# Optimization experiments

Hardware: AMD Instinct MI355X
Metric: run time of the kernel (lower is better)

Reference implementation:

```python
import jax, jax.numpy as jnp
import numpy as np

N, E, IN, H, D = 50000, 800000, 128, 2, 64  # heads=2, head_dim=64, hidden*2 = 128


def setup_inputs() -> dict:
    key = jax.random.key(0)
    ks = jax.random.split(key, 8)
    s = 1.0 / np.sqrt(IN)
    return {
        "x": jax.random.normal(ks[0], (N, IN), dtype=jnp.float32),
        "edge_index": jax.random.randint(ks[1], (2, E), 0, N, dtype=jnp.int64),
        "Wq": jax.random.normal(ks[2], (IN, H * D), dtype=jnp.float32) * s,
        "bq": jnp.zeros((H * D,), jnp.float32),
        "Wk": jax.random.normal(ks[3], (IN, H * D), dtype=jnp.float32) * s,
        "bk": jnp.zeros((H * D,), jnp.float32),
        "Wv": jax.random.normal(ks[4], (IN, H * D), dtype=jnp.float32) * s,
        "bv": jnp.zeros((H * D,), jnp.float32),
        "Wskip": jax.random.normal(ks[5], (IN, H * D), dtype=jnp.float32) * s,
        "bskip": jnp.zeros((H * D,), jnp.float32),
        "Wdec": jax.random.normal(ks[6], (H * D, IN), dtype=jnp.float32) * (1.0 / np.sqrt(H * D)),
        "bdec": jnp.zeros((IN,), jnp.float32),
    }


def reference(x, edge_index, Wq, bq, Wk, bk, Wv, bv, Wskip, bskip, Wdec, bdec):
    n = x.shape[0]
    src, dst = edge_index[0], edge_index[1]  # message flows src -> dst (PyG convention)
    q = (x @ Wq + bq).reshape(n, H, D)
    k = (x @ Wk + bk).reshape(n, H, D)
    v = (x @ Wv + bv).reshape(n, H, D)
    # per-edge multi-head scores [E, H]
    score = jnp.einsum('ehd,ehd->eh', q[dst], k[src]) / jnp.sqrt(jnp.asarray(D, x.dtype))
    # segment softmax over in-edges of each destination node
    m = jax.ops.segment_max(score, dst, num_segments=n)
    m = jnp.where(jnp.isfinite(m), m, jnp.zeros_like(m))  # nodes with no in-edges
    e = jnp.exp(score - m[dst])
    denom = jax.ops.segment_sum(e, dst, num_segments=n) + 1e-16
    alpha = e / denom[dst]                      # [E, H]
    msg = v[src] * alpha[..., None]             # [E, H, D]
    agg = jax.ops.segment_sum(msg, dst, num_segments=n)  # [N, H, D]
    z = agg.reshape(n, H * D) + (x @ Wskip + bskip)       # concat heads + root skip
    x_hat = z @ Wdec + bdec
    return (x_hat, z)
```

## Files before the change

### kernel.cpp

```cpp
#include <hip/hip_runtime.h>
#include <hip/hip_bf16.h>
#include <math.h>

typedef unsigned short u16;
typedef unsigned char u8;
typedef unsigned int u32;
typedef __attribute__((ext_vector_type(8))) short bf16x8;
typedef __attribute__((ext_vector_type(4))) float f32x4;

__device__ __forceinline__ float b2f(u16 u) {
  union { unsigned int i; float f; } x; x.i = ((unsigned int)u) << 16; return x.f;
}
__device__ __forceinline__ u16 f2b(float f) {
  union { float f; unsigned int i; } x; x.f = f;
  unsigned int r = x.i + 0x7FFFu + ((x.i >> 16) & 1u);
  return (u16)(r >> 16);
}
__device__ __forceinline__ float4 cvt4(ushort4 u) {
  return make_float4(b2f(u.x), b2f(u.y), b2f(u.z), b2f(u.w));
}
__device__ __forceinline__ float4 i8x4_to_f4(u32 w) {
  return make_float4((float)((int)(w << 24) >> 24), (float)((int)(w << 16) >> 24),
                     (float)((int)(w << 8) >> 24), (float)((int)w >> 24));
}

#if __has_builtin(__builtin_amdgcn_sdot4)
__device__ __forceinline__ int dot4i8(u32 a, u32 b) {
  return __builtin_amdgcn_sdot4((int)a, (int)b, 0, false);
}
#else
__device__ __forceinline__ int dot4i8(u32 a, u32 b) {
  int s = ((int)(a << 24) >> 24) * ((int)(b << 24) >> 24);
  s += ((int)(a << 16) >> 24) * ((int)(b << 16) >> 24);
  s += ((int)(a << 8) >> 24) * ((int)(b << 8) >> 24);
  s += ((int)a >> 24) * ((int)b >> 24);
  return s;
}
#endif

__device__ __forceinline__ bool ei_is_i64(const int* __restrict__ ei) {
  return (ei[1] | ei[3] | ei[5] | ei[7] | ei[9] | ei[11] | ei[13] | ei[15]) == 0;
}

__global__ __launch_bounds__(256) void wprep_kernel(
    const float* __restrict__ Wq, const float* __restrict__ Wk,
    const float* __restrict__ Wv, const float* __restrict__ Wsk,
    const float* __restrict__ Wd,
    const float* __restrict__ bq, const float* __restrict__ bk,
    const float* __restrict__ bv, const float* __restrict__ bsk,
    const float* __restrict__ bd,
    short* __restrict__ Wt, float* __restrict__ bias,
    int* __restrict__ cnt, int n) {
  int g = blockIdx.x * 256 + threadIdx.x;
  if (g < 5 * 16384) {
    int mat = g >> 14, rem = g & 16383;
    int nn = rem >> 7, kk = rem & 127;
    const float* W = (mat == 0) ? Wq : (mat == 1) ? Wk : (mat == 2) ? Wv
                     : (mat == 3) ? Wsk : Wd;
    float scl = (mat == 0) ? 0.125f : 1.f;
    Wt[g] = (short)f2b(W[kk * 128 + nn] * scl);
  }
  if (g < 5 * 128) {
    int mat = g >> 7, nn = g & 127;
    const float* B = (mat == 0) ? bq : (mat == 1) ? bk : (mat == 2) ? bv
                     : (mat == 3) ? bsk : bd;
    bias[g] = B[nn] * ((mat == 0) ? 0.125f : 1.f);
  }
  if (g < n) cnt[g] = 0;
}

__global__ __launch_bounds__(256) void count_kernel(const int* __restrict__ ei,
                                                    int* __restrict__ cnt,
                                                    u8* __restrict__ rank, int E) {
  int e = blockIdx.x * 256 + threadIdx.x;
  bool f = ei_is_i64(ei);
  if (e < E) {
    int idx = f ? (e << 1) : e;
    int dbase = f ? (E << 1) : E;
    int d = ei[dbase + idx];
    rank[e] = (u8)atomicAdd(&cnt[d], 1);
  }
}

__global__ __launch_bounds__(1024) void scanA_kernel(const int* __restrict__ cnt,
                                                     int* __restrict__ offs,
                                                     int* __restrict__ parts, int n) {
  __shared__ int wsum[16];
  int i = blockIdx.x * 1024 + threadIdx.x;
  int lane = threadIdx.x & 63, wid = threadIdx.x >> 6;
  int v = (i < n) ? cnt[i] : 0;
  int s = v;
#pragma unroll
  for (int off = 1; off < 64; off <<= 1) {
    int t = __shfl_up(s, off, 64);
    if (lane >= off) s += t;
  }
  if (lane == 63) wsum[wid] = s;
  __syncthreads();
  if (threadIdx.x == 0) {
    int acc = 0;
#pragma unroll
    for (int w = 0; w < 16; ++w) { int t = wsum[w]; wsum[w] = acc; acc += t; }
    parts[blockIdx.x] = acc;
  }
  __syncthreads();
  if (i < n) offs[i] = wsum[wid] + (s - v);
}

__global__ __launch_bounds__(1024) void scanC_kernel(int* __restrict__ offs,
                                                     const int* __restrict__ parts,
                                                     int n, int nb) {
  __shared__ int sh[2];
  if (threadIdx.x < 64) {
    int lane = threadIdx.x;
    int v = (lane < nb) ? parts[lane] : 0;
    int s = v;
#pragma unroll
    for (int off = 1; off < 64; off <<= 1) {
      int t = __shfl_up(s, off, 64);
      if (lane >= off) s += t;
    }
    int base = __shfl(s - v, blockIdx.x, 64);
    int tot  = __shfl(s, nb - 1, 64);
    if (lane == 0) { sh[0] = base; sh[1] = tot; }
  }
  __syncthreads();
  int i = blockIdx.x * 1024 + threadIdx.x;
  if (i < n) offs[i] += sh[0];
  if (i == 0) offs[n] = sh[1];
}

__global__ __launch_bounds__(256) void scatter_kernel(const int* __restrict__ ei,
                                                      const int* __restrict__ offs,
                                                      const u8* __restrict__ rank,
                                                      int* __restrict__ csr, int E) {
  int e = blockIdx.x * 256 + threadIdx.x;
  bool f = ei_is_i64(ei);
  if (e < E) {
    int idx = f ? (e << 1) : e;
    int dbase = f ? (E << 1) : E;
    int s = ei[idx];
    int d = ei[dbase + idx];
    int pos = offs[d] + (int)rank[e];
    __builtin_nontemporal_store(s, &csr[pos]);
  }
}

__global__ __launch_bounds__(256) void proj_kernel(const float* __restrict__ x,
    const short* __restrict__ Wt, const float* __restrict__ bias,
    u32* __restrict__ q8, float* __restrict__ qscb,
    u32* __restrict__ kvq, float* __restrict__ scb,
    u16* __restrict__ skipb, int n) {
  __shared__ short xt[32 * 128];
  int m0 = blockIdx.x * 32;
  int tid = threadIdx.x;
#pragma unroll
  for (int p = 0; p < 2; ++p) {
    int cid = tid + p * 256;
    int row = cid >> 4, c = cid & 15;
    int grow = m0 + row;
    bf16x8 val;
    if (grow < n) {
      const float* sp = x + (size_t)grow * 128 + c * 8;
      float4 f0 = *(const float4*)sp;
      float4 f1 = *(const float4*)(sp + 4);
      val[0] = (short)f2b(f0.x); val[1] = (short)f2b(f0.y);
      val[2] = (short)f2b(f0.z); val[3] = (short)f2b(f0.w);
      val[4] = (short)f2b(f1.x); val[5] = (short)f2b(f1.y);
      val[6] = (short)f2b(f1.z); val[7] = (short)f2b(f1.w);
    } else {
#pragma unroll
      for (int j = 0; j < 8; ++j) val[j] = 0;
    }
    *(bf16x8*)&xt[row * 128 + ((c ^ (row & 15)) << 3)] = val;
  }
  __syncthreads();

  int wid = tid >> 6, l = tid & 63;
  int lm = l & 15, lk = l >> 4;
  const short* W = Wt + (size_t)wid * 16384;
  f32x4 acc[2][8];
#pragma unroll
  for (int mt = 0; mt < 2; ++mt)
#pragma unroll
    for (int nt = 0; nt < 8; ++nt) acc[mt][nt] = (f32x4){0.f, 0.f, 0.f, 0.f};

#pragma unroll
  for (int s = 0; s < 4; ++s) {
    bf16x8 bfrag[2];
#pragma unroll
    for (int mt = 0; mt < 2; ++mt) {
      int ml = mt * 16 + lm;
      int c = s * 4 + lk;
      bfrag[mt] = *(const bf16x8*)&xt[ml * 128 + ((c ^ (ml & 15)) << 3)];
    }
#pragma unroll
    for (int nt = 0; nt < 8; ++nt) {
      bf16x8 afrag = *(const bf16x8*)(W + (size_t)(nt * 16 + lm) * 128 + s * 32 + lk * 8);
      acc[0][nt] = __builtin_amdgcn_mfma_f32_16x16x32_bf16(afrag, bfrag[0], acc[0][nt], 0, 0, 0);
      acc[1][nt] = __builtin_amdgcn_mfma_f32_16x16x32_bf16(afrag, bfrag[1], acc[1][nt], 0, 0, 0);
    }
  }

  const float* bs = bias + wid * 128;
  if (wid < 3) {
#pragma unroll
    for (int mt = 0; mt < 2; ++mt) {
      int m = m0 + mt * 16 + lm;
#pragma unroll
      for (int nt = 0; nt < 8; ++nt) {
        float4 b4 = *(const float4*)(bs + nt * 16 + lk * 4);
        acc[mt][nt][0] += b4.x; acc[mt][nt][1] += b4.y;
        acc[mt][nt][2] += b4.z; acc[mt][nt][3] += b4.w;
      }
#pragma unroll
      for (int h = 0; h < 2; ++h) {
        float am = 0.f;
#pragma unroll
        for (int nt4 = 0; nt4 < 4; ++nt4) {
          int nt = h * 4 + nt4;
#pragma unroll
          for (int j = 0; j < 4; ++j) am = fmaxf(am, fabsf(acc[mt][nt][j]));
        }
        am = fmaxf(am, __shfl_xor(am, 16));
        am = fmaxf(am, __shfl_xor(am, 32));
        float inv = (am > 0.f) ? 127.f / am : 0.f;
        if (m < n) {
#pragma unroll
          for (int nt4 = 0; nt4 < 4; ++nt4) {
            int nt = h * 4 + nt4;
            u32 pk = 0;
#pragma unroll
            for (int j = 0; j < 4; ++j) {
              float qv = fminf(fmaxf(rintf(acc[mt][nt][j] * inv), -127.f), 127.f);
              pk |= ((u32)((int)qv & 0xff)) << (8 * j);
            }
            int slot = nt4 * 4 + lk;
            if (wid == 0) q8[(size_t)m * 32 + h * 16 + slot] = pk;
            else kvq[(size_t)m * 64 + h * 32 + slot * 2 + (wid - 1)] = pk;
          }
          if (lk == 0) {
            float sc = am * (1.f / 127.f);
            if (wid == 0) qscb[(size_t)m * 2 + h] = sc;
            else scb[(size_t)m * 4 + h * 2 + (wid - 1)] = sc;
          }
        }
      }
    }
  } else {
#pragma unroll
    for (int mt = 0; mt < 2; ++mt) {
      int m = m0 + mt * 16 + lm;
      if (m >= n) continue;
#pragma unroll
      for (int nt = 0; nt < 8; ++nt) {
        int n4 = nt * 16 + lk * 4;
        float4 b4 = *(const float4*)(bs + n4);
        f32x4 a = acc[mt][nt];
        ushort4 o;
        o.x = f2b(a[0] + b4.x); o.y = f2b(a[1] + b4.y);
        o.z = f2b(a[2] + b4.z); o.w = f2b(a[3] + b4.w);
        *(ushort4*)(skipb + (size_t)m * 128 + n4) = o;
      }
    }
  }
}

__global__ __launch_bounds__(256) void dec_kernel(const float* __restrict__ zin,
    const short* __restrict__ Wt, const float* __restrict__ bias,
    float* __restrict__ out, int n) {
  __shared__ short zt[128 * 128];
  int m0 = blockIdx.x * 128;
  int tid = threadIdx.x;
#pragma unroll
  for (int p = 0; p < 8; ++p) {
    int cid = tid + p * 256;
    int row = cid >> 4, c = cid & 15;
    int grow = m0 + row;
    bf16x8 val;
    if (grow < n) {
      const float* sp = zin + (size_t)grow * 128 + c * 8;
      float4 f0 = *(const float4*)sp;
      float4 f1 = *(const float4*)(sp + 4);
      val[0] = (short)f2b(f0.x); val[1] = (short)f2b(f0.y);
      val[2] = (short)f2b(f0.z); val[3] = (short)f2b(f0.w);
      val[4] = (short)f2b(f1.x); val[5] = (short)f2b(f1.y);
      val[6] = (short)f2b(f1.z); val[7] = (short)f2b(f1.w);
    } else {
#pragma unroll
      for (int j = 0; j < 8; ++j) val[j] = 0;
    }
    *(bf16x8*)&zt[row * 128 + ((c ^ (row & 15)) << 3)] = val;
  }
  __syncthreads();

  int wid = tid >> 6, l = tid & 63;
  int lm = l & 15, lk = l >> 4;
  int mbase = wid * 32;
  f32x4 acc[2][8];
#pragma unroll
  for (int mt = 0; mt < 2; ++mt)
#pragma unroll
    for (int nt = 0; nt < 8; ++nt) acc[mt][nt] = (f32x4){0.f, 0.f, 0.f, 0.f};

#pragma unroll
  for (int s = 0; s < 4; ++s) {
    bf16x8 bfrag[2];
#pragma unroll
    for (int mt = 0; mt < 2; ++mt) {
      int ml = mbase + mt * 16 + lm;
      int c = s * 4 + lk;
      bfrag[mt] = *(const bf16x8*)&zt[ml * 128 + ((c ^ (ml & 15)) << 3)];
    }
#pragma unroll
    for (int nt = 0; nt < 8; ++nt) {
      bf16x8 afrag = *(const bf16x8*)(Wt + (size_t)(nt * 16 + lm) * 128 + s * 32 + lk * 8);
      acc[0][nt] = __builtin_amdgcn_mfma_f32_16x16x32_bf16(afrag, bfrag[0], acc[0][nt], 0, 0, 0);
      acc[1][nt] = __builtin_amdgcn_mfma_f32_16x16x32_bf16(afrag, bfrag[1], acc[1][nt], 0, 0, 0);
    }
  }

#pragma unroll
  for (int mt = 0; mt < 2; ++mt) {
    int m = m0 + mbase + mt * 16 + lm;
    if (m >= n) continue;
#pragma unroll
    for (int nt = 0; nt < 8; ++nt) {
      int n4 = nt * 16 + lk * 4;
      float4 b4 = *(const float4*)(bias + n4);
      f32x4 a = acc[mt][nt];
      *(float4*)(out + (size_t)m * 128 + n4) =
          make_float4(a[0] + b4.x, a[1] + b4.y, a[2] + b4.z, a[3] + b4.w);
    }
  }
}

#define EDGE_BODY(J, SACC, AACC)                                             \
  {                                                                          \
    int pi = dot4i8(qw, x##J.x);                                             \
    pi += __shfl_xor(pi, 1, 16);                                             \
    pi += __shfl_xor(pi, 2, 16);                                             \
    pi += __shfl_xor(pi, 4, 16);                                             \
    pi += __shfl_xor(pi, 8, 16);                                             \
    float w = __expf((float)pi * (qs * c##J.x));                             \
    float4 vv = i8x4_to_f4(x##J.y);                                          \
    float wv = w * c##J.y;                                                   \
    SACC += w;                                                               \
    AACC.x += wv * vv.x; AACC.y += wv * vv.y;                                \
    AACC.z += wv * vv.z; AACC.w += wv * vv.w;                                \
  }

__global__ __launch_bounds__(256) void attn_kernel(const u32* __restrict__ q8,
                                                   const float* __restrict__ qscb,
                                                   const u32* __restrict__ kvq,
                                                   const float* __restrict__ scb,
                                                   const u16* __restrict__ skipb,
                                                   const int* __restrict__ offs,
                                                   const int* __restrict__ csr,
                                                   float* __restrict__ z, int nn) {
  int dst = blockIdx.x * 8 + (threadIdx.x >> 5);
  int lane32 = threadIdx.x & 31;
  int h = lane32 >> 4, l16 = lane32 & 15;
  if (dst >= nn) return;
  u32 qw = q8[(size_t)dst * 32 + h * 16 + l16];
  float qs = qscb[(size_t)dst * 2 + h];
  int i0 = offs[dst], i1 = offs[dst + 1];
  int kvbase = h * 32 + l16 * 2;
  int scbase = h * 2;

  float s0 = 0.f, s1 = 0.f, s2 = 0.f, s3 = 0.f;
  float4 A0 = {0, 0, 0, 0}, A1 = {0, 0, 0, 0}, A2 = {0, 0, 0, 0}, A3 = {0, 0, 0, 0};

  int i = i0;
  for (; i + 7 < i1; i += 8) {
    int e0 = csr[i], e1 = csr[i + 1], e2 = csr[i + 2], e3 = csr[i + 3];
    int e4 = csr[i + 4], e5 = csr[i + 5], e6 = csr[i + 6], e7 = csr[i + 7];
    uint2 x0 = *(const uint2*)(kvq + (size_t)e0 * 64 + kvbase);
    uint2 x1 = *(const uint2*)(kvq + (size_t)e1 * 64 + kvbase);
    uint2 x2 = *(const uint2*)(kvq + (size_t)e2 * 64 + kvbase);
    uint2 x3 = *(const uint2*)(kvq + (size_t)e3 * 64 + kvbase);
    uint2 x4 = *(const uint2*)(kvq + (size_t)e4 * 64 + kvbase);
    uint2 x5 = *(const uint2*)(kvq + (size_t)e5 * 64 + kvbase);
    uint2 x6 = *(const uint2*)(kvq + (size_t)e6 * 64 + kvbase);
    uint2 x7 = *(const uint2*)(kvq + (size_t)e7 * 64 + kvbase);
    float2 c0 = *(const float2*)(scb + (size_t)e0 * 4 + scbase);
    float2 c1 = *(const float2*)(scb + (size_t)e1 * 4 + scbase);
    float2 c2 = *(const float2*)(scb + (size_t)e2 * 4 + scbase);
    float2 c3 = *(const float2*)(scb + (size_t)e3 * 4 + scbase);
    float2 c4 = *(const float2*)(scb + (size_t)e4 * 4 + scbase);
    float2 c5 = *(const float2*)(scb + (size_t)e5 * 4 + scbase);
    float2 c6 = *(const float2*)(scb + (size_t)e6 * 4 + scbase);
    float2 c7 = *(const float2*)(scb + (size_t)e7 * 4 + scbase);
    EDGE_BODY(0, s0, A0) EDGE_BODY(1, s1, A1)
    EDGE_BODY(2, s2, A2) EDGE_BODY(3, s3, A3)
    EDGE_BODY(4, s0, A0) EDGE_BODY(5, s1, A1)
    EDGE_BODY(6, s2, A2) EDGE_BODY(7, s3, A3)
  }
  if (i + 3 < i1) {
    int e0 = csr[i], e1 = csr[i + 1], e2 = csr[i + 2], e3 = csr[i + 3];
    i += 4;
    uint2 x0 = *(const uint2*)(kvq + (size_t)e0 * 64 + kvbase);
    uint2 x1 = *(const uint2*)(kvq + (size_t)e1 * 64 + kvbase);
    uint2 x2 = *(const uint2*)(kvq + (size_t)e2 * 64 + kvbase);
    uint2 x3 = *(const uint2*)(kvq + (size_t)e3 * 64 + kvbase);
    float2 c0 = *(const float2*)(scb + (size_t)e0 * 4 + scbase);
    float2 c1 = *(const float2*)(scb + (size_t)e1 * 4 + scbase);
    float2 c2 = *(const float2*)(scb + (size_t)e2 * 4 + scbase);
    float2 c3 = *(const float2*)(scb + (size_t)e3 * 4 + scbase);
    EDGE_BODY(0, s0, A0) EDGE_BODY(1, s1, A1)
    EDGE_BODY(2, s2, A2) EDGE_BODY(3, s3, A3)
  }
  for (; i < i1; ++i) {
    int e0 = csr[i];
    uint2 x0 = *(const uint2*)(kvq + (size_t)e0 * 64 + kvbase);
    float2 c0 = *(const float2*)(scb + (size_t)e0 * 4 + scbase);
    EDGE_BODY(0, s0, A0)
  }

  float sum = (s0 + s1) + (s2 + s3);
  float b0 = (A0.x + A1.x) + (A2.x + A3.x);
  float b1 = (A0.y + A1.y) + (A2.y + A3.y);
  float b2 = (A0.z + A1.z) + (A2.z + A3.z);
  float b3 = (A0.w + A1.w) + (A2.w + A3.w);
  float inv = 1.f / (sum + 1e-16f);
  int qoff = dst * 128 + h * 64 + l16 * 4;
  float4 sk = cvt4(*(const ushort4*)(skipb + qoff));
  *(float4*)(z + qoff) = make_float4(b0 * inv + sk.x, b1 * inv + sk.y,
                                     b2 * inv + sk.z, b3 * inv + sk.w);
}

extern "C" void kernel_launch(void* const* d_in, const int* in_sizes, int n_in,
                              void* d_out, int out_size, void* d_ws, size_t ws_size,
                              hipStream_t stream) {
  const float* x  = (const float*)d_in[0];
  const int*   ei = (const int*)d_in[1];
  const float* Wq = (const float*)d_in[2];
  const float* bq = (const float*)d_in[3];
  const float* Wk = (const float*)d_in[4];
  const float* bk = (const float*)d_in[5];
  const float* Wv = (const float*)d_in[6];
  const float* bv = (const float*)d_in[7];
  const float* Wsk = (const float*)d_in[8];
  const float* bsk = (const float*)d_in[9];
  const float* Wd = (const float*)d_in[10];
  const float* bd = (const float*)d_in[11];

  int N = in_sizes[0] / 128;
  int E = in_sizes[1] / 2;

  char* w = (char*)d_ws;
  auto alloc = [&](size_t bytes) {
    char* p = w;
    w += (bytes + 255) & ~(size_t)255;
    return p;
  };
  u32* q8    = (u32*)alloc((size_t)N * 32 * 4);
  float* qscb = (float*)alloc((size_t)N * 2 * 4);
  u32* kvq   = (u32*)alloc((size_t)N * 64 * 4);
  float* scb = (float*)alloc((size_t)N * 4 * 4);
  u16* skipb = (u16*)alloc((size_t)N * 128 * 2);
  int* cnt  = (int*)alloc((size_t)(N + 1) * 4);
  int* offs = (int*)alloc((size_t)(N + 1) * 4);
  u8*  rank = (u8*)alloc((size_t)E);
  int* csr  = (int*)alloc((size_t)E * 4);
  int* parts = (int*)alloc(66 * 4);
  short* Wt = (short*)alloc(5 * 16384 * 2);
  float* bias = (float*)alloc(5 * 128 * 4);

  float* xhat = (float*)d_out;
  float* z = xhat + (size_t)N * 128;

  int nb = (N + 1023) / 1024;

  wprep_kernel<<<320, 256, 0, stream>>>(Wq, Wk, Wv, Wsk, Wd, bq, bk, bv, bsk, bd,
                                        Wt, bias, cnt, N);
  count_kernel<<<(E + 255) / 256, 256, 0, stream>>>(ei, cnt, rank, E);
  scanA_kernel<<<nb, 1024, 0, stream>>>(cnt, offs, parts, N);
  scanC_kernel<<<nb, 1024, 0, stream>>>(offs, parts, N, nb);
  scatter_kernel<<<(E + 255) / 256, 256, 0, stream>>>(ei, offs, rank, csr, E);

  proj_kernel<<<(N + 31) / 32, 256, 0, stream>>>(x, Wt, bias, q8, qscb, kvq, scb,
                                                 skipb, N);

  attn_kernel<<<(N + 7) / 8, 256, 0, stream>>>(q8, qscb, kvq, scb, skipb, offs, csr,
                                               z, N);

  dec_kernel<<<(N + 127) / 128, 256, 0, stream>>>(z, Wt + 4 * 16384, bias + 4 * 128,
                                                  xhat, N);
}
```

Measured before the change: 193.3 us.

## Assign one wavefront per destination node with half-waves processing alternate edges

The attention kernel now gives each 64-lane wavefront one destination node instead of packing two nodes per wave. Each 32-lane half processes a different edge of each pair, and the halves combine their partial sums with a cross-half shuffle before the first half writes the output. Edge offsets are made wave-uniform with readfirstlane and addressing switches to 32-bit byte offsets. This removes divergence between two nodes with different degrees sharing a wave, at the cost of twice as many waves, an extra reduction step, and half the lanes idling on odd edge tails.

```diff
diff --git a/kernel.cpp b/kernel.cpp
--- a/kernel.cpp
+++ b/kernel.cpp
@@ -335,19 +335,23 @@
   }
 }
 
-#define EDGE_BODY(J, SACC, AACC)                                             \
+#define PAIR_BODY(EA, EB, SACC, AACC, HM)                                    \
   {                                                                          \
-    int pi = dot4i8(qw, x##J.x);                                             \
-    pi += __shfl_xor(pi, 1, 16);                                             \
-    pi += __shfl_xor(pi, 2, 16);                                             \
-    pi += __shfl_xor(pi, 4, 16);                                             \
-    pi += __shfl_xor(pi, 8, 16);                                             \
-    float w = __expf((float)pi * (qs * c##J.x));                             \
-    float4 vv = i8x4_to_f4(x##J.y);                                          \
-    float wv = w * c##J.y;                                                   \
-    SACC += w;                                                               \
-    AACC.x += wv * vv.x; AACC.y += wv * vv.y;                                \
-    AACC.z += wv * vv.z; AACC.w += wv * vv.w;                                \
+    int e_ = half ? (EB) : (EA);                                             \
+    u32 kvoff_ = (u32)e_ * 256u + (u32)(l32 * 8);                            \
+    uint2 kv_ = *(const uint2*)(kvbytes + kvoff_);                           \
+    float2 sc_ = *(const float2*)(scbytes + (u32)e_ * 16u + (u32)(h * 8));   \
+    int pi_ = dot4i8(qw, kv_.x);                                             \
+    pi_ += __shfl_xor(pi_, 1);                                               \
+    pi_ += __shfl_xor(pi_, 2);                                               \
+    pi_ += __shfl_xor(pi_, 4);                                               \
+    pi_ += __shfl_xor(pi_, 8);                                               \
+    float w_ = __expf((float)pi_ * (qs * sc_.x)) * (HM);                     \
+    float4 vv_ = i8x4_to_f4(kv_.y);                                          \
+    float wv_ = w_ * sc_.y;                                                  \
+    SACC += w_;                                                              \
+    AACC.x += wv_ * vv_.x; AACC.y += wv_ * vv_.y;                            \
+    AACC.z += wv_ * vv_.z; AACC.w += wv_ * vv_.w;                            \
   }
 
 __global__ __launch_bounds__(256) void attn_kernel(const u32* __restrict__ q8,
@@ -358,15 +362,20 @@
                                                    const int* __restrict__ offs,
                                                    const int* __restrict__ csr,
                                                    float* __restrict__ z, int nn) {
-  int dst = blockIdx.x * 8 + (threadIdx.x >> 5);
-  int lane32 = threadIdx.x & 31;
-  int h = lane32 >> 4, l16 = lane32 & 15;
+  int wv = __builtin_amdgcn_readfirstlane((int)(threadIdx.x >> 6));
+  int dst = blockIdx.x * 4 + wv;
   if (dst >= nn) return;
-  u32 qw = q8[(size_t)dst * 32 + h * 16 + l16];
+  int lane = threadIdx.x & 63;
+  int half = lane >> 5;
+  int l32 = lane & 31;
+  int h = l32 >> 4;
+  u32 qw = q8[(size_t)dst * 32 + l32];
   float qs = qscb[(size_t)dst * 2 + h];
-  int i0 = offs[dst], i1 = offs[dst + 1];
-  int kvbase = h * 32 + l16 * 2;
-  int scbase = h * 2;
+  int i0 = __builtin_amdgcn_readfirstlane(offs[dst]);
+  int i1 = __builtin_amdgcn_readfirstlane(offs[dst + 1]);
+  const u8* kvbytes = (const u8*)kvq;
+  const u8* scbytes = (const u8*)scb;
+  float hm1 = (half == 0) ? 1.f : 0.f;
 
   float s0 = 0.f, s1 = 0.f, s2 = 0.f, s3 = 0.f;
   float4 A0 = {0, 0, 0, 0}, A1 = {0, 0, 0, 0}, A2 = {0, 0, 0, 0}, A3 = {0, 0, 0, 0};
@@ -375,46 +384,18 @@
   for (; i + 7 < i1; i += 8) {
     int e0 = csr[i], e1 = csr[i + 1], e2 = csr[i + 2], e3 = csr[i + 3];
     int e4 = csr[i + 4], e5 = csr[i + 5], e6 = csr[i + 6], e7 = csr[i + 7];
-    uint2 x0 = *(const uint2*)(kvq + (size_t)e0 * 64 + kvbase);
-    uint2 x1 = *(const uint2*)(kvq + (size_t)e1 * 64 + kvbase);
-    uint2 x2 = *(const uint2*)(kvq + (size_t)e2 * 64 + kvbase);
-    uint2 x3 = *(const uint2*)(kvq + (size_t)e3 * 64 + kvbase);
-    uint2 x4 = *(const uint2*)(kvq + (size_t)e4 * 64 + kvbase);
-    uint2 x5 = *(const uint2*)(kvq + (size_t)e5 * 64 + kvbase);
-    uint2 x6 = *(const uint2*)(kvq + (size_t)e6 * 64 + kvbase);
-    uint2 x7 = *(const uint2*)(kvq + (size_t)e7 * 64 + kvbase);
-    float2 c0 = *(const float2*)(scb + (size_t)e0 * 4 + scbase);
-    float2 c1 = *(const float2*)(scb + (size_t)e1 * 4 + scbase);
-    float2 c2 = *(const float2*)(scb + (size_t)e2 * 4 + scbase);
-    float2 c3 = *(const float2*)(scb + (size_t)e3 * 4 + scbase);
-    float2 c4 = *(const float2*)(scb + (size_t)e4 * 4 + scbase);
-    float2 c5 = *(const float2*)(scb + (size_t)e5 * 4 + scbase);
-    float2 c6 = *(const float2*)(scb + (size_t)e6 * 4 + scbase);
-    float2 c7 = *(const float2*)(scb + (size_t)e7 * 4 + scbase);
-    EDGE_BODY(0, s0, A0) EDGE_BODY(1, s1, A1)
-    EDGE_BODY(2, s2, A2) EDGE_BODY(3, s3, A3)
-    EDGE_BODY(4, s0, A0) EDGE_BODY(5, s1, A1)
-    EDGE_BODY(6, s2, A2) EDGE_BODY(7, s3, A3)
-  }
-  if (i + 3 < i1) {
-    int e0 = csr[i], e1 = csr[i + 1], e2 = csr[i + 2], e3 = csr[i + 3];
-    i += 4;
-    uint2 x0 = *(const uint2*)(kvq + (size_t)e0 * 64 + kvbase);
-    uint2 x1 = *(const uint2*)(kvq + (size_t)e1 * 64 + kvbase);
-    uint2 x2 = *(const uint2*)(kvq + (size_t)e2 * 64 + kvbase);
-    uint2 x3 = *(const uint2*)(kvq + (size_t)e3 * 64 + kvbase);
-    float2 c0 = *(const float2*)(scb + (size_t)e0 * 4 + scbase);
-    float2 c1 = *(const float2*)(scb + (size_t)e1 * 4 + scbase);
-    float2 c2 = *(const float2*)(scb + (size_t)e2 * 4 + scbase);
-    float2 c3 = *(const float2*)(scb + (size_t)e3 * 4 + scbase);
-    EDGE_BODY(0, s0, A0) EDGE_BODY(1, s1, A1)
-    EDGE_BODY(2, s2, A2) EDGE_BODY(3, s3, A3)
-  }
-  for (; i < i1; ++i) {
+    PAIR_BODY(e0, e1, s0, A0, 1.f)
+    PAIR_BODY(e2, e3, s1, A1, 1.f)
+    PAIR_BODY(e4, e5, s2, A2, 1.f)
+    PAIR_BODY(e6, e7, s3, A3, 1.f)
+  }
+  for (; i + 1 < i1; i += 2) {
+    int e0 = csr[i], e1 = csr[i + 1];
+    PAIR_BODY(e0, e1, s0, A0, 1.f)
+  }
+  if (i < i1) {
     int e0 = csr[i];
-    uint2 x0 = *(const uint2*)(kvq + (size_t)e0 * 64 + kvbase);
-    float2 c0 = *(const float2*)(scb + (size_t)e0 * 4 + scbase);
-    EDGE_BODY(0, s0, A0)
+    PAIR_BODY(e0, e0, s0, A0, hm1)
   }
 
   float sum = (s0 + s1) + (s2 + s3);
@@ -422,11 +403,19 @@
   float b1 = (A0.y + A1.y) + (A2.y + A3.y);
   float b2 = (A0.z + A1.z) + (A2.z + A3.z);
   float b3 = (A0.w + A1.w) + (A2.w + A3.w);
-  float inv = 1.f / (sum + 1e-16f);
-  int qoff = dst * 128 + h * 64 + l16 * 4;
-  float4 sk = cvt4(*(const ushort4*)(skipb + qoff));
-  *(float4*)(z + qoff) = make_float4(b0 * inv + sk.x, b1 * inv + sk.y,
-                                     b2 * inv + sk.z, b3 * inv + sk.w);
+  sum += __shfl_xor(sum, 32);
+  b0 += __shfl_xor(b0, 32);
+  b1 += __shfl_xor(b1, 32);
+  b2 += __shfl_xor(b2, 32);
+  b3 += __shfl_xor(b3, 32);
+  if (half == 0) {
+    float inv = 1.f / (sum + 1e-16f);
+    int qoff = dst * 128 + l32 * 4;
+    qoff = dst * 128 + h * 64 + (l32 & 15) * 4;
+    float4 sk = cvt4(*(const ushort4*)(skipb + qoff));
+    *(float4*)(z + qoff) = make_float4(b0 * inv + sk.x, b1 * inv + sk.y,
+                                       b2 * inv + sk.z, b3 * inv + sk.w);
+  }
 }
 
 extern "C" void kernel_launch(void* const* d_in, const int* in_sizes, int n_in,
@@ -482,7 +471,7 @@
   proj_kernel<<<(N + 31) / 32, 256, 0, stream>>>(x, Wt, bias, q8, qscb, kvq, scb,
                                                  skipb, N);
 
-  attn_kernel<<<(N + 7) / 8, 256, 0, stream>>>(q8, qscb, kvq, scb, skipb, offs, csr,
+  attn_kernel<<<(N + 3) / 4, 256, 0, stream>>>(q8, qscb, kvq, scb, skipb, offs, csr,
                                                z, N);
 
   dec_kernel<<<(N + 127) / 128, 256, 0, stream>>>(z, Wt + 4 * 16384, bias + 4 * 128,
```

Result: faster. 179.6 us (-7.1%).
